# Kernel optimization log

Hardware: AMD Instinct MI355X
Metric: run time of the kernel (lower is better)

The kernel has to match this reference:

```python
import jax, jax.numpy as jnp
import numpy as np


def _unit(v):
    return v / jnp.linalg.norm(v, axis=-1, keepdims=True)


def setup_inputs() -> dict:
    key = jax.random.key(0)
    k1, k2, k3, k4 = jax.random.split(key, 4)
    N, M = 20000, 6890
    scan_vertices = jax.random.normal(k1, (1, N, 3), dtype=jnp.float32)
    template_vertices = jax.random.normal(k2, (1, M, 3), dtype=jnp.float32)
    # normals are unit vectors in practice
    scan_normals = _unit(jax.random.normal(k3, (N, 3), dtype=jnp.float32))
    template_normals = _unit(jax.random.normal(k4, (M, 3), dtype=jnp.float32))
    return {
        "scan_vertices": scan_vertices,
        "template_vertices": template_vertices,
        "scan_normals": scan_normals,
        "template_normals": template_normals,
        "K_knn": 15,
    }


def reference(scan_vertices, template_vertices, scan_normals, template_normals, K_knn):
    sv = scan_vertices.reshape(-1, 3)       # [N,3]
    tv = template_vertices.reshape(-1, 3)   # [M,3]
    # Brute-force pairwise distances [M,N] (vectorizes the per-vertex loop)
    dist = jnp.linalg.norm(sv[None, :, :] - tv[:, None, :], axis=-1)
    # NOTE: torch.topk defaults to largest=True, so the original selects the
    # K LARGEST distances. lax.top_k also returns the largest -> faithful.
    _, knn_idx = jax.lax.top_k(dist, K_knn)                 # [M,K]
    knn_normals = scan_normals[knn_idx]                     # [M,K,3]
    dot = jnp.sum(knn_normals * template_normals[:, None, :], axis=-1)  # [M,K]
    angle_deg = jnp.degrees(jnp.arccos(jnp.clip(dot, -1.0, 1.0)))
    best = jnp.argmin(angle_deg, axis=1)                    # [M]
    sel = jnp.take_along_axis(knn_idx, best[:, None], axis=1)[:, 0]  # [M]
    mse = jnp.mean(jnp.linalg.norm(sv[sel] - tv, axis=1))
    return mse
```

## Files before the change

### kernel.cpp

```cpp
#include <hip/hip_runtime.h>
#include <math.h>


constexpr int K = 15;
constexpr int NBUCK = 256;
constexpr int WAVES = 4;

__device__ __forceinline__ int bucket_of(float k2) {
    int b = (int)(k2 * 8.0f);
    b = b > (NBUCK - 1) ? (NBUCK - 1) : b;
    return (NBUCK - 1) - b;
}

__global__ __launch_bounds__(256) void hist_kernel(
    const float* __restrict__ sv, int* __restrict__ blkhist, int N)
{
    __shared__ int h[NBUCK];
    int t = threadIdx.x;
    h[t] = 0;
    __syncthreads();
    int i = blockIdx.x * 256 + t;
    if (i < N) {
        float x = sv[3*i], y = sv[3*i+1], z = sv[3*i+2];
        atomicAdd(&h[bucket_of(fmaf(x, x, fmaf(y, y, z*z)))], 1);
    }
    __syncthreads();
    blkhist[blockIdx.x * NBUCK + t] = h[t];
}

__global__ __launch_bounds__(256) void scan_scatter_kernel(
    const float* __restrict__ sv,
    const int*   __restrict__ blkhist,
    float4*      __restrict__ sorted,
    float*       __restrict__ smax,
    int N, int nb, int nblk)
{
    __shared__ int tmp[NBUCK];
    __shared__ int startSh[NBUCK];
    __shared__ int cursor[NBUCK];
    const int t   = threadIdx.x;
    const int blk = blockIdx.x;

    int mine = 0, total = 0;
#pragma unroll 8
    for (int b = 0; b < nblk; ++b) {
        int v = blkhist[b * NBUCK + t];
        if (b < blk) mine += v;
        total += v;
    }
    tmp[t] = total;
    __syncthreads();
    for (int d = 1; d < NBUCK; d <<= 1) {
        int u = (t >= d) ? tmp[t - d] : 0;
        __syncthreads();
        tmp[t] += u;
        __syncthreads();
    }
    int startv = tmp[t] - total;
    startSh[t] = startv;
    cursor[t]  = startv + mine;
    __syncthreads();

    if (blk == 0) {
        for (int j = t; j < nb; j += 256) {
            int pos = j * 64;
            int lo = 0, hi = NBUCK - 1;
            while (lo < hi) {
                int mid = (lo + hi + 1) >> 1;
                if (startSh[mid] <= pos) lo = mid; else hi = mid - 1;
            }
            int bOrig = (NBUCK - 1) - lo;
            smax[j] = sqrtf((float)(bOrig + 1) * 0.125f);
        }
    }

    int i = blk * 256 + t;
    if (i < N) {
        float x = sv[3*i], y = sv[3*i+1], z = sv[3*i+2];
        float k2 = fmaf(x, x, fmaf(y, y, z*z));
        int pos = atomicAdd(&cursor[bucket_of(k2)], 1);
        sorted[pos] = make_float4(x, y, z, __int_as_float(i));
    }
}

template<bool SORTED>
__global__ __launch_bounds__(WAVES * 64) void knn_loss_kernel(
    const float4* __restrict__ pts,
    const float*  __restrict__ smax,
    const float*  __restrict__ sv,
    const float*  __restrict__ tv,
    const float*  __restrict__ sn,
    const float*  __restrict__ tn,
    float* __restrict__ partial,
    int N, int M, float invM)
{
    __shared__ float bsum[WAVES];
    const int lane = threadIdx.x & 63;
    const int w    = threadIdx.x >> 6;
    const int m    = blockIdx.x * WAVES + w;
    const bool valid = (m < M);

    float contrib = 0.0f;
    if (valid) {
        const float tvx = tv[3*m], tvy = tv[3*m+1], tvz = tv[3*m+2];
        const float tlen = sqrtf(tvx*tvx + tvy*tvy + tvz*tvz);

        float v; int idx;
        {
            int l = (lane < N) ? lane : 0;
            float px, py, pz;
            if (SORTED) {
                float4 q = pts[l];
                px = q.x; py = q.y; pz = q.z; idx = __float_as_int(q.w);
            } else {
                px = sv[3*l]; py = sv[3*l+1]; pz = sv[3*l+2]; idx = l;
            }
            float dx = px - tvx, dy = py - tvy, dz = pz - tvz;
            v = fmaf(dx, dx, fmaf(dy, dy, dz * dz));
            if (lane >= N) { v = -1.0f; idx = 0x7FFFFFFF; }
        }
#pragma unroll
        for (int k = 2; k <= 64; k <<= 1) {
#pragma unroll
            for (int j = k >> 1; j > 0; j >>= 1) {
                float ov = __shfl_xor(v, j);
                int   oi = __shfl_xor(idx, j);
                bool up    = ((lane & k) == 0);
                bool lower = ((lane & j) == 0);
                bool mine  = (v > ov) || (v == ov && idx < oi);
                bool keep  = lower ? (up ? mine : !mine) : (up ? !mine : mine);
                if (!keep) { v = ov; idx = oi; }
            }
        }
        float eV = (lane < K) ? v : -1.0f;
        int   eI = idx;
        float thr = __shfl(v, K - 1);

        for (int ib = 64; ib < N; ib += 64) {
            int  i   = ib + lane;
            bool has = (i < N);
            float d2; int oi2;
            if (SORTED) {
                float4 q = pts[has ? i : 0];
                float bnd = smax[ib >> 6] + tlen;
                if (bnd * bnd * 1.00001f < thr) break;
                float dx = q.x - tvx, dy = q.y - tvy, dz = q.z - tvz;
                d2 = fmaf(dx, dx, fmaf(dy, dy, dz * dz));
                oi2 = __float_as_int(q.w);
            } else {
                int g = has ? i : 0;
                float dx = sv[3*g] - tvx, dy = sv[3*g+1] - tvy, dz = sv[3*g+2] - tvz;
                d2 = fmaf(dx, dx, fmaf(dy, dy, dz * dz));
                oi2 = i;
            }
            unsigned long long mb = __ballot(has && (d2 >= thr));
            while (mb) {
                int src = __ffsll(mb) - 1;
                mb &= mb - 1;
                float cv = __shfl(d2, src);
                int   ci = __shfl(oi2, src);
                unsigned long long bb =
                    __ballot((eV > cv) || (eV == cv && eI < ci)) & 0x7FFFull;
                int p = __popcll(bb);
                if (p < K) {
                    float uv = __shfl_up(eV, 1);
                    int   ui = __shfl_up(eI, 1);
                    if (lane < K) {
                        if (lane == p)      { eV = cv; eI = ci; }
                        else if (lane > p)  { eV = uv; eI = ui; }
                    }
                    thr = __shfl(eV, K - 1);
                    if (mb) mb &= __ballot(d2 >= thr);
                }
            }
        }

        const float tnx = tn[3*m], tny = tn[3*m+1], tnz = tn[3*m+2];
        float ang = 3.0e38f;
        int myI = eI;
        if (lane < K && myI != 0x7FFFFFFF) {
            float dot = sn[3*myI]*tnx + sn[3*myI+1]*tny + sn[3*myI+2]*tnz;
            dot = fminf(1.0f, fmaxf(-1.0f, dot));
            ang = acosf(dot) * 57.29577951308232f;
        }
        float ba = ang; int br = lane; int bi = myI;
#pragma unroll
        for (int s = 1; s < 16; s <<= 1) {
            float oa  = __shfl_xor(ba, s);
            int   orr = __shfl_xor(br, s);
            int   oi  = __shfl_xor(bi, s);
            bool take = (oa < ba) || (oa == ba && orr < br);
            if (take) { ba = oa; br = orr; bi = oi; }
        }
        if (lane == 0) {
            float dx = sv[3*bi]   - tvx;
            float dy = sv[3*bi+1] - tvy;
            float dz = sv[3*bi+2] - tvz;
            contrib = sqrtf(dx*dx + dy*dy + dz*dz) * invM;
        }
    }

    if (lane == 0) bsum[w] = contrib;
    __syncthreads();
    if (threadIdx.x == 0)
        partial[blockIdx.x] = bsum[0] + bsum[1] + bsum[2] + bsum[3];
}

__global__ __launch_bounds__(256) void reduce_kernel(
    const float* __restrict__ partial, float* __restrict__ out, int n)
{
    __shared__ float sh[4];
    const int lane = threadIdx.x & 63;
    const int w    = threadIdx.x >> 6;
    float s = 0.0f;
    for (int i = threadIdx.x; i < n; i += 256) s += partial[i];
#pragma unroll
    for (int d = 1; d < 64; d <<= 1) s += __shfl_xor(s, d);
    if (lane == 0) sh[w] = s;
    __syncthreads();
    if (threadIdx.x == 0) out[0] = sh[0] + sh[1] + sh[2] + sh[3];
}

extern "C" void kernel_launch(void* const* d_in, const int* in_sizes, int n_in,
                              void* d_out, int out_size, void* d_ws, size_t ws_size,
                              hipStream_t stream) {
    const float* sv = (const float*)d_in[0];
    const float* tv = (const float*)d_in[1];
    const float* sn = (const float*)d_in[2];
    const float* tn = (const float*)d_in[3];

    int N = in_sizes[0] / 3;
    int M = in_sizes[1] / 3;
    int nb = (N + 63) / 64;
    float* out = (float*)d_out;
    float invM = 1.0f / (float)M;
    int grid  = (M + WAVES - 1) / WAVES;
    int nblk  = (N + 255) / 256;

    size_t offSorted  = 0;
    size_t offSmax    = offSorted + (size_t)N * sizeof(float4);
    size_t offHist    = (offSmax + (size_t)nb * sizeof(float) + 15) & ~(size_t)15;
    size_t offPartial = offHist + (size_t)nblk * NBUCK * sizeof(int);
    size_t need       = offPartial + (size_t)grid * sizeof(float);

    if (ws_size >= need) {
        float4* sorted  = (float4*)((char*)d_ws + offSorted);
        float*  smax    = (float*) ((char*)d_ws + offSmax);
        int*    blkhist = (int*)   ((char*)d_ws + offHist);
        float*  partial = (float*) ((char*)d_ws + offPartial);

        hist_kernel        <<<nblk, 256, 0, stream>>>(sv, blkhist, N);
        scan_scatter_kernel<<<nblk, 256, 0, stream>>>(sv, blkhist, sorted,
                                                      smax, N, nb, nblk);
        knn_loss_kernel<true><<<grid, WAVES * 64, 0, stream>>>(
            sorted, smax, sv, tv, sn, tn, partial, N, M, invM);
        reduce_kernel      <<<1, 256, 0, stream>>>(partial, out, grid);
    } else if (ws_size >= (size_t)grid * sizeof(float)) {
        float* partial = (float*)d_ws;
        knn_loss_kernel<false><<<grid, WAVES * 64, 0, stream>>>(
            nullptr, nullptr, sv, tv, sn, tn, partial, N, M, invM);
        reduce_kernel      <<<1, 256, 0, stream>>>(partial, out, grid);
    }
}
```

Before: 30.52 us.

## Bucket scan points by radius and octant, cull chunks with bounding boxes

Bucketing now keys on a coarser squared-radius shell combined with the sign octant. The scatter pass records a per-64-point chunk axis-aligned bounding box using atomic min/max on order-preserving encoded floats. The KNN loop skips any chunk whose farthest possible distance cannot beat the current K-th largest threshold. It still breaks early on the radius bound. This aims to avoid loading and evaluating chunks that cannot contribute, at the cost of extra global atomics in scatter, metadata initialization, and coarser radius bounds.

Result: slower. 48.90 us (+60.2%).

```diff
diff --git a/kernel.cpp b/kernel.cpp
--- a/kernel.cpp
+++ b/kernel.cpp
@@ -3,37 +3,58 @@
 
 
 constexpr int K = 15;
+constexpr int NSH = 32;
 constexpr int NBUCK = 256;
 constexpr int WAVES = 4;
 
-__device__ __forceinline__ int bucket_of(float k2) {
-    int b = (int)(k2 * 8.0f);
-    b = b > (NBUCK - 1) ? (NBUCK - 1) : b;
-    return (NBUCK - 1) - b;
+__device__ __forceinline__ int bucket_of(float x, float y, float z) {
+    float k2 = fmaf(x, x, fmaf(y, y, z * z));
+    int b = (k2 >= (float)(NSH - 1)) ? (NSH - 1) : (int)k2;
+    int fb = (NSH - 1) - b;
+    int o = (x < 0.0f ? 1 : 0) | (y < 0.0f ? 2 : 0) | (z < 0.0f ? 4 : 0);
+    return (fb << 3) | o;
+}
+__device__ __forceinline__ unsigned encf(float f) {
+    unsigned b = __float_as_uint(f);
+    return (b >> 31) ? ~b : (b | 0x80000000u);
+}
+__device__ __forceinline__ float decf(unsigned u) {
+    return (u >> 31) ? __uint_as_float(u ^ 0x80000000u)
+                     : __uint_as_float(~u);
 }
 
 __global__ __launch_bounds__(256) void hist_kernel(
-    const float* __restrict__ sv, int* __restrict__ blkhist, int N)
+    const float* __restrict__ sv, int* __restrict__ blkhist,
+    unsigned* __restrict__ metaA, unsigned* __restrict__ metaB,
+    int N, int nmeta, int nblk)
 {
     __shared__ int h[NBUCK];
-    int t = threadIdx.x;
+    const int t = threadIdx.x;
     h[t] = 0;
     __syncthreads();
     int i = blockIdx.x * 256 + t;
     if (i < N) {
         float x = sv[3*i], y = sv[3*i+1], z = sv[3*i+2];
-        atomicAdd(&h[bucket_of(fmaf(x, x, fmaf(y, y, z*z)))], 1);
+        atomicAdd(&h[bucket_of(x, y, z)], 1);
     }
     __syncthreads();
     blkhist[blockIdx.x * NBUCK + t] = h[t];
+    if (t < 32) {
+        int s = t & 7;
+        for (int c = blockIdx.x * 4 + (t >> 3); c < nmeta; c += nblk * 4) {
+            if (s < 4) metaA[c*4 + s]       = (s == 0) ? 0u : 0xFFFFFFFFu;
+            else       metaB[c*4 + (s - 4)] = 0u;
+        }
+    }
 }
 
 __global__ __launch_bounds__(256) void scan_scatter_kernel(
     const float* __restrict__ sv,
     const int*   __restrict__ blkhist,
     float4*      __restrict__ sorted,
-    float*       __restrict__ smax,
-    int N, int nb, int nblk)
+    unsigned*    __restrict__ metaA,
+    unsigned*    __restrict__ metaB,
+    int N, int ncha, int nblk)
 {
     __shared__ int tmp[NBUCK];
     __shared__ int startSh[NBUCK];
@@ -62,37 +83,45 @@
     __syncthreads();
 
     if (blk == 0) {
-        for (int j = t; j < nb; j += 256) {
-            int pos = j * 64;
-            int lo = 0, hi = NBUCK - 1;
+        for (int c = t; c < ncha; c += 256) {
+            int pos = c * 64;
+            int lo = 0, hi = NSH - 1;
             while (lo < hi) {
                 int mid = (lo + hi + 1) >> 1;
-                if (startSh[mid] <= pos) lo = mid; else hi = mid - 1;
-            }
-            int bOrig = (NBUCK - 1) - lo;
-            smax[j] = sqrtf((float)(bOrig + 1) * 0.125f);
+                if (startSh[mid << 3] <= pos) lo = mid; else hi = mid - 1;
+            }
+            float r = (lo == 0) ? 3.0e38f : sqrtf((float)(NSH - lo));
+            metaA[c*4] = __float_as_uint(r);
         }
     }
 
     int i = blk * 256 + t;
     if (i < N) {
         float x = sv[3*i], y = sv[3*i+1], z = sv[3*i+2];
-        float k2 = fmaf(x, x, fmaf(y, y, z*z));
-        int pos = atomicAdd(&cursor[bucket_of(k2)], 1);
+        int b = bucket_of(x, y, z);
+        int pos = atomicAdd(&cursor[b], 1);
         sorted[pos] = make_float4(x, y, z, __int_as_float(i));
+        int c = pos >> 6;
+        atomicMin(&metaA[c*4 + 1], encf(x));
+        atomicMin(&metaA[c*4 + 2], encf(y));
+        atomicMin(&metaA[c*4 + 3], encf(z));
+        atomicMax(&metaB[c*4 + 1], encf(x));
+        atomicMax(&metaB[c*4 + 2], encf(y));
+        atomicMax(&metaB[c*4 + 3], encf(z));
     }
 }
 
 template<bool SORTED>
 __global__ __launch_bounds__(WAVES * 64) void knn_loss_kernel(
-    const float4* __restrict__ pts,
-    const float*  __restrict__ smax,
-    const float*  __restrict__ sv,
-    const float*  __restrict__ tv,
-    const float*  __restrict__ sn,
-    const float*  __restrict__ tn,
+    const float4*   __restrict__ pts,
+    const unsigned* __restrict__ metaA,
+    const unsigned* __restrict__ metaB,
+    const float*    __restrict__ sv,
+    const float*    __restrict__ tv,
+    const float*    __restrict__ sn,
+    const float*    __restrict__ tn,
     float* __restrict__ partial,
-    int N, int M, float invM)
+    int N, int M, float invM, int ncha)
 {
     __shared__ float bsum[WAVES];
     const int lane = threadIdx.x & 63;
@@ -136,41 +165,79 @@
         int   eI = idx;
         float thr = __shfl(v, K - 1);
 
-        for (int ib = 64; ib < N; ib += 64) {
-            int  i   = ib + lane;
-            bool has = (i < N);
-            float d2; int oi2;
-            if (SORTED) {
-                float4 q = pts[has ? i : 0];
-                float bnd = smax[ib >> 6] + tlen;
+        if (SORTED) {
+            const uint4* mA4 = (const uint4*)metaA;
+            const uint4* mB4 = (const uint4*)metaB;
+            uint4 mA = mA4[1], mB = mB4[1];
+            for (int c = 1; c < ncha; ++c) {
+                float smaxc = __uint_as_float(mA.x);
+                float bnd = smaxc + tlen;
                 if (bnd * bnd * 1.00001f < thr) break;
-                float dx = q.x - tvx, dy = q.y - tvy, dz = q.z - tvz;
-                d2 = fmaf(dx, dx, fmaf(dy, dy, dz * dz));
-                oi2 = __float_as_int(q.w);
-            } else {
+                uint4 mAn = mA4[c + 1], mBn = mB4[c + 1];
+                float lx = decf(mA.y), ly = decf(mA.z), lz = decf(mA.w);
+                float hx = decf(mB.y), hy = decf(mB.z), hz = decf(mB.w);
+                float ax = fmaxf((lx-tvx)*(lx-tvx), (hx-tvx)*(hx-tvx));
+                float ay = fmaxf((ly-tvy)*(ly-tvy), (hy-tvy)*(hy-tvy));
+                float az = fmaxf((lz-tvz)*(lz-tvz), (hz-tvz)*(hz-tvz));
+                float bmax2 = ax + ay + az;
+                if (bmax2 * 1.00001f >= thr) {
+                    int  i   = c * 64 + lane;
+                    bool has = (i < N);
+                    float4 q = pts[has ? i : 0];
+                    float dx = q.x - tvx, dy = q.y - tvy, dz = q.z - tvz;
+                    float d2 = fmaf(dx, dx, fmaf(dy, dy, dz * dz));
+                    int oi2 = __float_as_int(q.w);
+                    unsigned long long mb = __ballot(has && (d2 >= thr));
+                    while (mb) {
+                        int src = __ffsll(mb) - 1;
+                        mb &= mb - 1;
+                        float cv = __shfl(d2, src);
+                        int   ci = __shfl(oi2, src);
+                        unsigned long long bb =
+                            __ballot((eV > cv) || (eV == cv && eI < ci)) & 0x7FFFull;
+                        int p = __popcll(bb);
+                        if (p < K) {
+                            float uv = __shfl_up(eV, 1);
+                            int   ui = __shfl_up(eI, 1);
+                            if (lane < K) {
+                                if (lane == p)      { eV = cv; eI = ci; }
+                                else if (lane > p)  { eV = uv; eI = ui; }
+                            }
+                            thr = __shfl(eV, K - 1);
+                            if (mb) mb &= __ballot(d2 >= thr);
+                        }
+                    }
+                }
+                mA = mAn; mB = mBn;
+            }
+        } else {
+            for (int ib = 64; ib < N; ib += 64) {
+                int  i   = ib + lane;
+                bool has = (i < N);
                 int g = has ? i : 0;
-                float dx = sv[3*g] - tvx, dy = sv[3*g+1] - tvy, dz = sv[3*g+2] - tvz;
-                d2 = fmaf(dx, dx, fmaf(dy, dy, dz * dz));
-                oi2 = i;
-            }
-            unsigned long long mb = __ballot(has && (d2 >= thr));
-            while (mb) {
-                int src = __ffsll(mb) - 1;
-                mb &= mb - 1;
-                float cv = __shfl(d2, src);
-                int   ci = __shfl(oi2, src);
-                unsigned long long bb =
-                    __ballot((eV > cv) || (eV == cv && eI < ci)) & 0x7FFFull;
-                int p = __popcll(bb);
-                if (p < K) {
-                    float uv = __shfl_up(eV, 1);
-                    int   ui = __shfl_up(eI, 1);
-                    if (lane < K) {
-                        if (lane == p)      { eV = cv; eI = ci; }
-                        else if (lane > p)  { eV = uv; eI = ui; }
+                float dx = sv[3*g] - tvx, dy = sv[3*g+1] - tvy,
+                      dz = sv[3*g+2] - tvz;
+                float d2 = fmaf(dx, dx, fmaf(dy, dy, dz * dz));
+                int oi2 = i;
+                unsigned long long mb = __ballot(has && (d2 >= thr));
+                while (mb) {
+                    int src = __ffsll(mb) - 1;
+                    mb &= mb - 1;
+                    float cv = __shfl(d2, src);
+                    int   ci = __shfl(oi2, src);
+                    unsigned long long bb =
+                        __ballot((eV > cv) || (eV == cv && eI < ci)) & 0x7FFFull;
+                    int p = __popcll(bb);
+                    if (p < K) {
+                        float uv = __shfl_up(eV, 1);
+                        int   ui = __shfl_up(eI, 1);
+                        if (lane < K) {
+                            if (lane == p)      { eV = cv; eI = ci; }
+                            else if (lane > p)  { eV = uv; eI = ui; }
+                        }
+                        thr = __shfl(eV, K - 1);
+                        if (mb) mb &= __ballot(d2 >= thr);
                     }
-                    thr = __shfl(eV, K - 1);
-                    if (mb) mb &= __ballot(d2 >= thr);
                 }
             }
         }
@@ -231,34 +298,39 @@
 
     int N = in_sizes[0] / 3;
     int M = in_sizes[1] / 3;
-    int nb = (N + 63) / 64;
+    int ncha  = (N + 63) / 64;
+    int nmeta = ncha + 1;
     float* out = (float*)d_out;
     float invM = 1.0f / (float)M;
     int grid  = (M + WAVES - 1) / WAVES;
     int nblk  = (N + 255) / 256;
 
     size_t offSorted  = 0;
-    size_t offSmax    = offSorted + (size_t)N * sizeof(float4);
-    size_t offHist    = (offSmax + (size_t)nb * sizeof(float) + 15) & ~(size_t)15;
+    size_t offMetaA   = offSorted + (size_t)N * sizeof(float4);
+    size_t offMetaB   = offMetaA + (size_t)nmeta * 4 * sizeof(unsigned);
+    size_t offHist    = offMetaB + (size_t)nmeta * 4 * sizeof(unsigned);
     size_t offPartial = offHist + (size_t)nblk * NBUCK * sizeof(int);
     size_t need       = offPartial + (size_t)grid * sizeof(float);
 
     if (ws_size >= need) {
-        float4* sorted  = (float4*)((char*)d_ws + offSorted);
-        float*  smax    = (float*) ((char*)d_ws + offSmax);
-        int*    blkhist = (int*)   ((char*)d_ws + offHist);
-        float*  partial = (float*) ((char*)d_ws + offPartial);
-
-        hist_kernel        <<<nblk, 256, 0, stream>>>(sv, blkhist, N);
+        float4*   sorted  = (float4*)  ((char*)d_ws + offSorted);
+        unsigned* metaA   = (unsigned*)((char*)d_ws + offMetaA);
+        unsigned* metaB   = (unsigned*)((char*)d_ws + offMetaB);
+        int*      blkhist = (int*)     ((char*)d_ws + offHist);
+        float*    partial = (float*)   ((char*)d_ws + offPartial);
+
+        hist_kernel        <<<nblk, 256, 0, stream>>>(sv, blkhist, metaA,
+                                                      metaB, N, nmeta, nblk);
         scan_scatter_kernel<<<nblk, 256, 0, stream>>>(sv, blkhist, sorted,
-                                                      smax, N, nb, nblk);
+                                                      metaA, metaB,
+                                                      N, ncha, nblk);
         knn_loss_kernel<true><<<grid, WAVES * 64, 0, stream>>>(
-            sorted, smax, sv, tv, sn, tn, partial, N, M, invM);
+            sorted, metaA, metaB, sv, tv, sn, tn, partial, N, M, invM, ncha);
         reduce_kernel      <<<1, 256, 0, stream>>>(partial, out, grid);
     } else if (ws_size >= (size_t)grid * sizeof(float)) {
         float* partial = (float*)d_ws;
         knn_loss_kernel<false><<<grid, WAVES * 64, 0, stream>>>(
-            nullptr, nullptr, sv, tv, sn, tn, partial, N, M, invM);
-        reduce_kernel      <<<1, 256, 0, stream>>>(partial, out, grid);
-    }
-}
+            nullptr, nullptr, nullptr, sv, tv, sn, tn, partial, N, M, invM, ncha);
+        reduce_kernel<<<1, 256, 0, stream>>>(partial, out, grid);
+    }
+}
```
